# Optimization experiments

Hardware: AMD Instinct MI355X
Metric: run time of the kernel (lower is better)

## Reference

```python
import jax, jax.numpy as jnp
import numpy as np

N_NODES = 100000
N_EDGES = 3200000
IN_DIM, HID, N_LAB = 128, 64, 121


def setup_inputs() -> dict:
    key = jax.random.key(0)
    ks = jax.random.split(key, 8)
    x = jax.random.normal(ks[0], (N_NODES, IN_DIM), dtype=jnp.float32)
    edge_index = jax.random.randint(ks[1], (2, N_EDGES), 0, N_NODES, dtype=jnp.int64)
    W1 = jax.random.normal(ks[2], (IN_DIM, HID), dtype=jnp.float32) * (1.0 / np.sqrt(IN_DIM))
    b1 = jnp.zeros((HID,), dtype=jnp.float32)
    W2 = jax.random.normal(ks[3], (HID, HID), dtype=jnp.float32) * (1.0 / np.sqrt(HID))
    b2 = jnp.zeros((HID,), dtype=jnp.float32)
    Wout = jax.random.normal(ks[4], (HID, N_LAB), dtype=jnp.float32) * (1.0 / np.sqrt(HID))
    bout = jnp.zeros((N_LAB,), dtype=jnp.float32)
    return {"x": x, "edge_index": edge_index, "W1": W1, "b1": b1,
            "W2": W2, "b2": b2, "Wout": Wout, "bout": bout}


def _gcn_conv(x, W, b, src, dst, norm, n):
    # x' = D^{-1/2}(A+I)D^{-1/2} X W + b  (edges already include self-loops)
    xw = x @ W                                   # [N, out]
    msg = xw[src] * norm[:, None]                # [E+N, out] gather + scale
    agg = jax.ops.segment_sum(msg, dst, num_segments=n)  # scatter-add
    return agg + b


def reference(x, edge_index, W1, b1, W2, b2, Wout, bout):
    n = x.shape[0]
    loop = jnp.arange(n, dtype=edge_index.dtype)
    src = jnp.concatenate([edge_index[0], loop])
    dst = jnp.concatenate([edge_index[1], loop])
    # symmetric normalization (self-loops guarantee deg >= 1)
    deg = jax.ops.segment_sum(jnp.ones_like(dst, dtype=x.dtype), dst, num_segments=n)
    dinv = jax.lax.rsqrt(deg)
    norm = dinv[src] * dinv[dst]                 # [E+N]

    h = jax.nn.relu(_gcn_conv(x, W1, b1, src, dst, norm, n))
    # dropout p=0.5 is identity in eval mode (training=False)
    h = jax.nn.relu(_gcn_conv(h, W2, b2, src, dst, norm, n))
    logits = h @ Wout + bout                     # [N, num_labels]
    return logits
```

## Files before the change

kernel.cpp:

```cpp
#include <hip/hip_runtime.h>
#include <hip/hip_bf16.h>
#include <hip/hip_fp16.h>


#define IN_DIM 128
#define HID 64
#define N_LAB 121
#define NB_BLK 256

__global__ void scan1(const int* __restrict__ in, int* __restrict__ out,
                      int* __restrict__ bsums, int n) {
    __shared__ int s[256];
    int i = blockIdx.x * 256 + threadIdx.x;
    int v = (i < n) ? in[i] : 0;
    s[threadIdx.x] = v;
    __syncthreads();
    for (int off = 1; off < 256; off <<= 1) {
        int t = (threadIdx.x >= off) ? s[threadIdx.x - off] : 0;
        __syncthreads();
        s[threadIdx.x] += t;
        __syncthreads();
    }
    if (i < n) out[i] = s[threadIdx.x] - v;
    if (threadIdx.x == 255) bsums[blockIdx.x] = s[255];
}

__global__ void scan2(int* __restrict__ bsums, int nb) {
    __shared__ int s[512];
    int v = (threadIdx.x < nb) ? bsums[threadIdx.x] : 0;
    s[threadIdx.x] = v;
    __syncthreads();
    for (int off = 1; off < 512; off <<= 1) {
        int t = (threadIdx.x >= off) ? s[threadIdx.x - off] : 0;
        __syncthreads();
        s[threadIdx.x] += t;
        __syncthreads();
    }
    if (threadIdx.x < nb) bsums[threadIdx.x] = s[threadIdx.x] - v;
}

__global__ void scan_add(int* __restrict__ out, const int* __restrict__ bsums, int n) {
    int i = blockIdx.x * 256 + threadIdx.x;
    if (i < n) out[i] += bsums[blockIdx.x];
}

__global__ __launch_bounds__(256) void bucket_count(const int* __restrict__ dst,
                                                    int* __restrict__ counts,
                                                    int nbuk, int chunk, int E) {
    extern __shared__ int c[];
    for (int j = threadIdx.x; j < nbuk; j += 256) c[j] = 0;
    __syncthreads();
    int beg = blockIdx.x * chunk;
    int end = min(beg + chunk, E);
    for (int i = beg + threadIdx.x; i < end; i += 256)
        atomicAdd(&c[dst[i] >> 8], 1);
    __syncthreads();
    for (int j = threadIdx.x; j < nbuk; j += 256)
        counts[j * NB_BLK + blockIdx.x] = c[j];
}

__global__ __launch_bounds__(256) void bucket_scatter(const int* __restrict__ src,
                                                      const int* __restrict__ dst,
                                                      const int* __restrict__ base,
                                                      int* __restrict__ bucketed,
                                                      int nbuk, int chunk, int E) {
    extern __shared__ int c[];
    for (int j = threadIdx.x; j < nbuk; j += 256) c[j] = 0;
    __syncthreads();
    int beg = blockIdx.x * chunk;
    int end = min(beg + chunk, E);
    for (int i = beg + threadIdx.x; i < end; i += 256) {
        int d = dst[i];
        int b = d >> 8;
        int r = atomicAdd(&c[b], 1);
        int pos = base[b * NB_BLK + blockIdx.x] + r;
        bucketed[pos] = ((d & 255) << 17) | src[i];
    }
}

__global__ __launch_bounds__(256) void bucket_sort(const int* __restrict__ bucketed,
                                                   const int* __restrict__ base,
                                                   int* __restrict__ srcs,
                                                   int* __restrict__ row_ptr,
                                                   float* __restrict__ dinv,
                                                   int nbuk, int N, int E) {
    __shared__ int h[256];
    __shared__ int cur[256];
    int b = blockIdx.x;
    int nodeBase = b << 8;
    int s = base[b * NB_BLK];
    int e = (b == nbuk - 1) ? E : base[(b + 1) * NB_BLK];
    h[threadIdx.x] = 0;
    __syncthreads();
    for (int i = s + threadIdx.x; i < e; i += 256)
        atomicAdd(&h[bucketed[i] >> 17], 1);
    __syncthreads();
    int v = h[threadIdx.x];
    for (int off = 1; off < 256; off <<= 1) {
        int t = (threadIdx.x >= off) ? h[threadIdx.x - off] : 0;
        __syncthreads();
        h[threadIdx.x] += t;
        __syncthreads();
    }
    int excl = h[threadIdx.x] - v;
    cur[threadIdx.x] = excl;
    int node = nodeBase + threadIdx.x;
    if (node < N) {
        row_ptr[node] = s + excl;
        dinv[node] = rsqrtf((float)v + 1.0f);
    }
    if (b == nbuk - 1 && threadIdx.x == 0) row_ptr[N] = E;
    __syncthreads();
    for (int i = s + threadIdx.x; i < e; i += 256) {
        int p = bucketed[i];
        int d = p >> 17;
        int r = atomicAdd(&cur[d], 1);
        srcs[s + r] = p & 0x1FFFF;
    }
}

template <int K, int N, typename OT>
__global__ __launch_bounds__(256) void gemm_kernel(
        const float* __restrict__ A, const float* __restrict__ B,
        const float* __restrict__ bias, const float* __restrict__ rowscale,
        OT* __restrict__ C, int M) {
    constexpr int ROWS = 64;
    constexpr int NPAD = (N <= 64) ? 64 : 128;
    constexpr int CG = NPAD / 4;
    constexpr int RG = 256 / CG;
    constexpr int RPT = ROWS / RG;
    __shared__ float Bs[K * NPAD];
    __shared__ float As[ROWS * K];

    for (int i = threadIdx.x; i < K * NPAD; i += 256) {
        int c = i & (NPAD - 1);
        int k = i / NPAD;
        Bs[i] = (c < N) ? B[k * N + c] : 0.f;
    }
    const int row_base = blockIdx.x * ROWS;
    const float* Ablk = A + (size_t)row_base * K;
    int avail = (M - row_base) * K;
    if (avail > ROWS * K) avail = ROWS * K;
    const int nvec = avail >> 2;
    const float4* __restrict__ Av = (const float4*)Ablk;
    float4* Asv = (float4*)As;
    for (int i = threadIdx.x; i < nvec; i += 256) Asv[i] = Av[i];
    __syncthreads();

    const int cg = threadIdx.x % CG;
    const int rg = threadIdx.x / CG;

    float acc[RPT][4];
    #pragma unroll
    for (int j = 0; j < RPT; ++j) {
        acc[j][0] = 0.f; acc[j][1] = 0.f; acc[j][2] = 0.f; acc[j][3] = 0.f;
    }

    for (int k = 0; k < K; k += 4) {
        float4 Bq[4];
        #pragma unroll
        for (int kk = 0; kk < 4; ++kk)
            Bq[kk] = *(const float4*)&Bs[(k + kk) * NPAD + cg * 4];
        #pragma unroll
        for (int j = 0; j < RPT; ++j) {
            const float4 Aq = *(const float4*)&As[(rg + RG * j) * K + k];
            #pragma unroll
            for (int c = 0; c < 4; ++c) {
                const float b0 = ((const float*)&Bq[0])[c];
                const float b1 = ((const float*)&Bq[1])[c];
                const float b2 = ((const float*)&Bq[2])[c];
                const float b3 = ((const float*)&Bq[3])[c];
                float a = acc[j][c];
                a = fmaf(Aq.x, b0, a);
                a = fmaf(Aq.y, b1, a);
                a = fmaf(Aq.z, b2, a);
                a = fmaf(Aq.w, b3, a);
                acc[j][c] = a;
            }
        }
    }

    float bv[4];
    #pragma unroll
    for (int c = 0; c < 4; ++c) {
        int col = cg * 4 + c;
        bv[c] = (bias && col < N) ? bias[col] : 0.f;
    }

    #pragma unroll
    for (int j = 0; j < RPT; ++j) {
        const int r = row_base + rg + RG * j;
        if (r >= M) continue;
        const float sc = rowscale ? rowscale[r] : 1.0f;
        float o[4];
        #pragma unroll
        for (int c = 0; c < 4; ++c) o[c] = fmaf(acc[j][c], sc, bv[c]);
        OT* Crow = C + (size_t)r * N;
        if constexpr (sizeof(OT) == 4 && (N % 4 == 0)) {
            *(float4*)&Crow[cg * 4] = make_float4(o[0], o[1], o[2], o[3]);
        } else if constexpr (sizeof(OT) == 2 && (N % 4 == 0)) {
            __half2* p = (__half2*)&Crow[cg * 4];
            p[0] = __floats2half2_rn(o[0], o[1]);
            p[1] = __floats2half2_rn(o[2], o[3]);
        } else {
            #pragma unroll
            for (int c = 0; c < 4; ++c) {
                int col = cg * 4 + c;
                if (col < N) Crow[col] = (OT)o[c];
            }
        }
    }
}

__global__ __launch_bounds__(256) void aggregate(
        const __half* __restrict__ feat2, const int* __restrict__ rp,
        const int* __restrict__ srcs, const float* __restrict__ dinv,
        const float* __restrict__ bias, float* __restrict__ out, int N) {
    size_t gid = (size_t)blockIdx.x * blockDim.x + threadIdx.x;
    int r = (int)(gid >> 6);
    int f = (int)(gid & 63);
    if (r >= N) return;
    int beg = rp[r], end = rp[r + 1];
    float acc = __half2float(feat2[((size_t)r << 6) + f]);
    int e = beg;
    for (; e + 8 <= end; e += 8) {
        int s0 = srcs[e], s1 = srcs[e + 1], s2 = srcs[e + 2], s3 = srcs[e + 3];
        int s4 = srcs[e + 4], s5 = srcs[e + 5], s6 = srcs[e + 6], s7 = srcs[e + 7];
        float v0 = __half2float(feat2[((size_t)s0 << 6) + f]);
        float v1 = __half2float(feat2[((size_t)s1 << 6) + f]);
        float v2 = __half2float(feat2[((size_t)s2 << 6) + f]);
        float v3 = __half2float(feat2[((size_t)s3 << 6) + f]);
        float v4 = __half2float(feat2[((size_t)s4 << 6) + f]);
        float v5 = __half2float(feat2[((size_t)s5 << 6) + f]);
        float v6 = __half2float(feat2[((size_t)s6 << 6) + f]);
        float v7 = __half2float(feat2[((size_t)s7 << 6) + f]);
        acc += v0; acc += v1; acc += v2; acc += v3;
        acc += v4; acc += v5; acc += v6; acc += v7;
    }
    for (; e < end; ++e) acc += __half2float(feat2[((size_t)srcs[e] << 6) + f]);
    out[gid] = fmaxf(fmaf(acc, dinv[r], bias[f]), 0.f);
}

extern "C" void kernel_launch(void* const* d_in, const int* in_sizes, int n_in,
                              void* d_out, int out_size, void* d_ws, size_t ws_size,
                              hipStream_t stream) {
    const float* x    = (const float*)d_in[0];
    const int*   ei   = (const int*)d_in[1];
    const float* W1   = (const float*)d_in[2];
    const float* b1   = (const float*)d_in[3];
    const float* W2   = (const float*)d_in[4];
    const float* b2   = (const float*)d_in[5];
    const float* Wout = (const float*)d_in[6];
    const float* bout = (const float*)d_in[7];
    float* out = (float*)d_out;

    const int N = in_sizes[0] / IN_DIM;
    const int E = in_sizes[1] / 2;
    const int* srcI = ei;
    const int* dstI = ei + E;

    const int nbuk = (N + 255) >> 8;
    const int M1 = nbuk * NB_BLK;
    const int chunk = (E + NB_BLK - 1) / NB_BLK;

    int*    row_ptr = (int*)d_ws;
    float*  dinv    = (float*)(row_ptr + (N + 1));
    int*    counts  = (int*)(dinv + N);
    int*    base    = counts + M1;
    int*    bsums2  = base + M1;
    int*    srcs    = bsums2 + 512;
    __half* feat2   = (__half*)(srcs + E);
    float*  hbuf    = (float*)(feat2 + (size_t)N * HID);
    int*    bucketed = (int*)feat2;

    const int nbM = (M1 + 255) / 256;
    const int gemmBlocks = (N + 63) / 64;
    const int aggBlocks = (int)(((size_t)N * HID + 255) / 256);
    const size_t ldsBuk = (size_t)nbuk * sizeof(int);

    bucket_count<<<NB_BLK, 256, ldsBuk, stream>>>(dstI, counts, nbuk, chunk, E);
    scan1<<<nbM, 256, 0, stream>>>(counts, base, bsums2, M1);
    scan2<<<1, 512, 0, stream>>>(bsums2, nbM);
    scan_add<<<nbM, 256, 0, stream>>>(base, bsums2, M1);
    bucket_scatter<<<NB_BLK, 256, ldsBuk, stream>>>(srcI, dstI, base, bucketed, nbuk, chunk, E);
    bucket_sort<<<nbuk, 256, 0, stream>>>(bucketed, base, srcs, row_ptr, dinv, nbuk, N, E);

    gemm_kernel<IN_DIM, HID, __half><<<gemmBlocks, 256, 0, stream>>>(x, W1, nullptr, dinv, feat2, N);
    aggregate<<<aggBlocks, 256, 0, stream>>>(feat2, row_ptr, srcs, dinv, b1, hbuf, N);

    gemm_kernel<HID, HID, __half><<<gemmBlocks, 256, 0, stream>>>(hbuf, W2, nullptr, dinv, feat2, N);
    aggregate<<<aggBlocks, 256, 0, stream>>>(feat2, row_ptr, srcs, dinv, b2, hbuf, N);

    gemm_kernel<HID, N_LAB, float><<<gemmBlocks, 256, 0, stream>>>(hbuf, Wout, bout, nullptr, out, N);
}
```

Baseline: 548.0 us.

## Restructure aggregation: 8 edges per wavefront with 16-byte vector gathers and shuffle reduce

The aggregate kernel now assigns one 64-lane wavefront per node, split into 8 slots of 8 lanes. Each slot handles a different edge and loads 8 half features with a single 16-byte load, where before each lane loaded one 2-byte half per edge. Partial sums are combined across slots with xor shuffles, and one slot writes the results as float4. The feat2 buffer is aligned to 16 bytes so the vector loads are legal. The aim is fewer, wider memory transactions and more edges in flight. The cost is the cross-lane reduction and idle lanes on low-degree tails.

```diff
diff --git a/kernel.cpp b/kernel.cpp
--- a/kernel.cpp
+++ b/kernel.cpp
@@ -216,29 +216,77 @@
         const __half* __restrict__ feat2, const int* __restrict__ rp,
         const int* __restrict__ srcs, const float* __restrict__ dinv,
         const float* __restrict__ bias, float* __restrict__ out, int N) {
-    size_t gid = (size_t)blockIdx.x * blockDim.x + threadIdx.x;
-    int r = (int)(gid >> 6);
-    int f = (int)(gid & 63);
-    if (r >= N) return;
-    int beg = rp[r], end = rp[r + 1];
-    float acc = __half2float(feat2[((size_t)r << 6) + f]);
+    const int wid = (int)((((size_t)blockIdx.x * 256) + threadIdx.x) >> 6);
+    if (wid >= N) return;
+    const int lane = threadIdx.x & 63;
+    const int slot = lane >> 3;
+    const int oct  = lane & 7;
+    const size_t fbase = (size_t)oct << 3;
+
+    float acc[8];
+    #pragma unroll
+    for (int i = 0; i < 8; ++i) acc[i] = 0.f;
+
+    if (slot == 0) {
+        const uint4 raw = *(const uint4*)(feat2 + (((size_t)wid << 6) + fbase));
+        const __half2* h = (const __half2*)&raw;
+        #pragma unroll
+        for (int i = 0; i < 4; ++i) {
+            const float2 f = __half22float2(h[i]);
+            acc[2 * i]     += f.x;
+            acc[2 * i + 1] += f.y;
+        }
+    }
+
+    const int beg = rp[wid], end = rp[wid + 1];
     int e = beg;
-    for (; e + 8 <= end; e += 8) {
-        int s0 = srcs[e], s1 = srcs[e + 1], s2 = srcs[e + 2], s3 = srcs[e + 3];
-        int s4 = srcs[e + 4], s5 = srcs[e + 5], s6 = srcs[e + 6], s7 = srcs[e + 7];
-        float v0 = __half2float(feat2[((size_t)s0 << 6) + f]);
-        float v1 = __half2float(feat2[((size_t)s1 << 6) + f]);
-        float v2 = __half2float(feat2[((size_t)s2 << 6) + f]);
-        float v3 = __half2float(feat2[((size_t)s3 << 6) + f]);
-        float v4 = __half2float(feat2[((size_t)s4 << 6) + f]);
-        float v5 = __half2float(feat2[((size_t)s5 << 6) + f]);
-        float v6 = __half2float(feat2[((size_t)s6 << 6) + f]);
-        float v7 = __half2float(feat2[((size_t)s7 << 6) + f]);
-        acc += v0; acc += v1; acc += v2; acc += v3;
-        acc += v4; acc += v5; acc += v6; acc += v7;
-    }
-    for (; e < end; ++e) acc += __half2float(feat2[((size_t)srcs[e] << 6) + f]);
-    out[gid] = fmaxf(fmaf(acc, dinv[r], bias[f]), 0.f);
+    for (; e + 16 <= end; e += 16) {
+        const int s0 = srcs[e + slot];
+        const int s1 = srcs[e + 8 + slot];
+        const uint4 r0 = *(const uint4*)(feat2 + (((size_t)s0 << 6) + fbase));
+        const uint4 r1 = *(const uint4*)(feat2 + (((size_t)s1 << 6) + fbase));
+        const __half2* h0 = (const __half2*)&r0;
+        const __half2* h1 = (const __half2*)&r1;
+        #pragma unroll
+        for (int i = 0; i < 4; ++i) {
+            const float2 f0 = __half22float2(h0[i]);
+            const float2 f1 = __half22float2(h1[i]);
+            acc[2 * i]     += f0.x + f1.x;
+            acc[2 * i + 1] += f0.y + f1.y;
+        }
+    }
+    for (; e < end; e += 8) {
+        const int idx = e + slot;
+        if (idx < end) {
+            const int s = srcs[idx];
+            const uint4 r0 = *(const uint4*)(feat2 + (((size_t)s << 6) + fbase));
+            const __half2* h0 = (const __half2*)&r0;
+            #pragma unroll
+            for (int i = 0; i < 4; ++i) {
+                const float2 f = __half22float2(h0[i]);
+                acc[2 * i]     += f.x;
+                acc[2 * i + 1] += f.y;
+            }
+        }
+    }
+
+    #pragma unroll
+    for (int m = 8; m <= 32; m <<= 1) {
+        #pragma unroll
+        for (int i = 0; i < 8; ++i)
+            acc[i] += __shfl_xor(acc[i], m, 64);
+    }
+
+    if (slot == 0) {
+        const float sc = dinv[wid];
+        float o[8];
+        #pragma unroll
+        for (int i = 0; i < 8; ++i)
+            o[i] = fmaxf(fmaf(acc[i], sc, bias[fbase + i]), 0.f);
+        float4* dst4 = (float4*)(out + (((size_t)wid << 6) + fbase));
+        dst4[0] = make_float4(o[0], o[1], o[2], o[3]);
+        dst4[1] = make_float4(o[4], o[5], o[6], o[7]);
+    }
 }
 
 extern "C" void kernel_launch(void* const* d_in, const int* in_sizes, int n_in,
@@ -269,7 +317,7 @@
     int*    base    = counts + M1;
     int*    bsums2  = base + M1;
     int*    srcs    = bsums2 + 512;
-    __half* feat2   = (__half*)(srcs + E);
+    __half* feat2   = (__half*)(((uintptr_t)(srcs + E) + 15) & ~(uintptr_t)15);
     float*  hbuf    = (float*)(feat2 + (size_t)N * HID);
     int*    bucketed = (int*)feat2;
 
```

Result: faster. 522.7 us (-4.6%).
